# Optimization experiments

Hardware: AMD Instinct MI355X
Metric: run time of the kernel (lower is better)

The kernel has to match this reference:

```python
import jax, jax.numpy as jnp
import numpy as np

BATCH, IN_F, OUT_F = 8192, 4096, 4096


def setup_inputs() -> dict:
    key = jax.random.key(0)
    kx, kw = jax.random.split(key)
    x = jax.random.normal(kx, (BATCH, IN_F), dtype=jnp.float32)
    # weights binarized to {-1, +1} as in __init__ (uniform(-1,1) then sign)
    W = jnp.where(jax.random.normal(kw, (OUT_F, IN_F)) > 0, 1.0, -1.0).astype(jnp.float32)
    return {"x": x, "W": W}


def reference(x, W):
    # forward: input thresholded to {0,1} (x>0 -> 1, else 0), then x_bin @ W^T, no bias
    x_bin = (x > 0).astype(x.dtype)
    return jnp.matmul(x_bin, W.T)  # [batch, out_features]
```

## Files before the change

kernel.cpp:

```cpp
#include <hip/hip_runtime.h>
#include <stdint.h>

typedef __attribute__((ext_vector_type(4))) int v4i;

#define BATCH 8192
#define KDIM  4096
#define NOUT  4096

__global__ __launch_bounds__(256) void pack_x(const float* __restrict__ x,
                                              uint32_t* __restrict__ xb) {
    int t = blockIdx.x * 256 + threadIdx.x;
    float4 f = ((const float4*)x)[t];
    uint32_t b = (f.x > 0.f ? 1u : 0u)
               | ((f.y > 0.f ? 1u : 0u) << 8)
               | ((f.z > 0.f ? 1u : 0u) << 16)
               | ((f.w > 0.f ? 1u : 0u) << 24);
    xb[t] = b;
}

__global__ __launch_bounds__(256) void pack_w(const float* __restrict__ w,
                                              uint32_t* __restrict__ wb) {
    int t = blockIdx.x * 256 + threadIdx.x;
    float4 f = ((const float4*)w)[t];
    uint32_t b = (f.x > 0.f ? 0x01u : 0xFFu)
               | ((f.y > 0.f ? 0x01u : 0xFFu) << 8)
               | ((f.z > 0.f ? 0x01u : 0xFFu) << 16)
               | ((f.w > 0.f ? 0x01u : 0xFFu) << 24);
    wb[t] = b;
}

__global__ __launch_bounds__(256) void bin_gemm(const int8_t* __restrict__ A,
                                                const int8_t* __restrict__ B,
                                                float* __restrict__ C) {
    __shared__ __align__(16) int8_t smA[128 * 64];
    __shared__ __align__(16) int8_t smB[128 * 64];

    const int tid  = threadIdx.x;
    const int w    = tid >> 6;
    const int lane = tid & 63;
    const int q    = lane >> 4;
    const int mp   = lane & 15;

    const int Mbase = blockIdx.y * 128;
    const int Nbase = blockIdx.x * 128;
    const int wm = (w >> 1) * 64;
    const int wn = (w & 1) * 64;

    const int srow = lane >> 2;
    const int swz  = ((lane & 3) ^ ((lane >> 3) & 3)) * 16;
    const int g0   = (w * 2 + 0) * 16;
    const int g1   = (w * 2 + 1) * 16;

    const int8_t* gA0 = A + (size_t)(Mbase + g0 + srow) * KDIM + swz;
    const int8_t* gA1 = A + (size_t)(Mbase + g1 + srow) * KDIM + swz;
    const int8_t* gB0 = B + (size_t)(Nbase + g0 + srow) * KDIM + swz;
    const int8_t* gB1 = B + (size_t)(Nbase + g1 + srow) * KDIM + swz;

    auto lA0 = (__attribute__((address_space(3))) void*)(smA + g0 * 64);
    auto lA1 = (__attribute__((address_space(3))) void*)(smA + g1 * 64);
    auto lB0 = (__attribute__((address_space(3))) void*)(smB + g0 * 64);
    auto lB1 = (__attribute__((address_space(3))) void*)(smB + g1 * 64);

    const int slot = (q ^ ((mp >> 1) & 3)) * 16;

    v4i acc[4][4] = {};

    for (int kt = 0; kt < KDIM / 64; ++kt) {
        const int kof = kt * 64;
        __builtin_amdgcn_global_load_lds(
            (__attribute__((address_space(1))) void*)(gA0 + kof), lA0, 16, 0, 0);
        __builtin_amdgcn_global_load_lds(
            (__attribute__((address_space(1))) void*)(gA1 + kof), lA1, 16, 0, 0);
        __builtin_amdgcn_global_load_lds(
            (__attribute__((address_space(1))) void*)(gB0 + kof), lB0, 16, 0, 0);
        __builtin_amdgcn_global_load_lds(
            (__attribute__((address_space(1))) void*)(gB1 + kof), lB1, 16, 0, 0);
        __syncthreads();

        v4i af[4], bf[4];
        #pragma unroll
        for (int i = 0; i < 4; ++i)
            af[i] = *(const v4i*)(smA + (wm + i * 16 + mp) * 64 + slot);
        #pragma unroll
        for (int i = 0; i < 4; ++i)
            bf[i] = *(const v4i*)(smB + (wn + i * 16 + mp) * 64 + slot);

        #pragma unroll
        for (int mi = 0; mi < 4; ++mi)
            #pragma unroll
            for (int ni = 0; ni < 4; ++ni)
                acc[mi][ni] = __builtin_amdgcn_mfma_i32_16x16x64_i8(
                    af[mi], bf[ni], acc[mi][ni], 0, 0, 0);
        __syncthreads();
    }

    float* Cp = C + (size_t)(Mbase + wm + q * 4) * NOUT + (Nbase + wn + mp);
    #pragma unroll
    for (int mi = 0; mi < 4; ++mi)
        #pragma unroll
        for (int ni = 0; ni < 4; ++ni)
            #pragma unroll
            for (int r = 0; r < 4; ++r)
                Cp[(size_t)(mi * 16 + r) * NOUT + ni * 16] = (float)acc[mi][ni][r];
}

extern "C" void kernel_launch(void* const* d_in, const int* in_sizes, int n_in,
                              void* d_out, int out_size, void* d_ws, size_t ws_size,
                              hipStream_t stream) {
    const float* x = (const float*)d_in[0];
    const float* W = (const float*)d_in[1];
    float* out = (float*)d_out;

    int8_t* xb = (int8_t*)d_ws;
    int8_t* wb = (int8_t*)d_ws + (size_t)BATCH * KDIM;

    pack_x<<<(BATCH * (size_t)KDIM / 4) / 256, 256, 0, stream>>>(x, (uint32_t*)xb);
    pack_w<<<((size_t)NOUT * KDIM / 4) / 256, 256, 0, stream>>>(W, (uint32_t*)wb);

    dim3 grid(NOUT / 128, BATCH / 128);
    bin_gemm<<<grid, 256, 0, stream>>>(xb, wb, out);
}
```

Measured before the change: 398.1 us.

## Switch binary GEMM from int8 MFMA to FP4 scaled MFMA with nibble packing

Inputs and weights are packed as 4-bit FP4 (E2M1) codes instead of int8: x becomes 1.0 or 0 and W becomes ±1.0. The GEMM uses the scaled f8f6f4 MFMA at 16x16x128 in FP4 mode with unit scales and an fp32 accumulator. This halves packed-operand bytes and doubles K per MFMA instruction, so the main loop runs half as many iterations. Exactness depends on fp32 accumulation of integer sums up to 4096, which stays exact, and on the nibble ordering matching what the MFMA expects for its operand layout.

```diff
diff --git a/kernel.cpp b/kernel.cpp
--- a/kernel.cpp
+++ b/kernel.cpp
@@ -1,39 +1,54 @@
 #include <hip/hip_runtime.h>
 #include <stdint.h>
 
-typedef __attribute__((ext_vector_type(4))) int v4i;
+typedef __attribute__((ext_vector_type(4))) int   v4i;
+typedef __attribute__((ext_vector_type(8))) int   v8i;
+typedef __attribute__((ext_vector_type(4))) float v4f;
 
 #define BATCH 8192
 #define KDIM  4096
 #define NOUT  4096
+#define KB    (KDIM / 2)
 
-__global__ __launch_bounds__(256) void pack_x(const float* __restrict__ x,
-                                              uint32_t* __restrict__ xb) {
+__global__ __launch_bounds__(256) void pack_x4(const float* __restrict__ x,
+                                               uint32_t* __restrict__ xb) {
     int t = blockIdx.x * 256 + threadIdx.x;
-    float4 f = ((const float4*)x)[t];
-    uint32_t b = (f.x > 0.f ? 1u : 0u)
-               | ((f.y > 0.f ? 1u : 0u) << 8)
-               | ((f.z > 0.f ? 1u : 0u) << 16)
-               | ((f.w > 0.f ? 1u : 0u) << 24);
+    const float4* p = (const float4*)x + (size_t)t * 2;
+    float4 f0 = p[0];
+    float4 f1 = p[1];
+    uint32_t b = (f0.x > 0.f ? 0x2u        : 0u)
+               | (f0.y > 0.f ? 0x20u       : 0u)
+               | (f0.z > 0.f ? 0x200u      : 0u)
+               | (f0.w > 0.f ? 0x2000u     : 0u)
+               | (f1.x > 0.f ? 0x20000u    : 0u)
+               | (f1.y > 0.f ? 0x200000u   : 0u)
+               | (f1.z > 0.f ? 0x2000000u  : 0u)
+               | (f1.w > 0.f ? 0x20000000u : 0u);
     xb[t] = b;
 }
 
-__global__ __launch_bounds__(256) void pack_w(const float* __restrict__ w,
-                                              uint32_t* __restrict__ wb) {
+__global__ __launch_bounds__(256) void pack_w4(const float* __restrict__ w,
+                                               uint32_t* __restrict__ wb) {
     int t = blockIdx.x * 256 + threadIdx.x;
-    float4 f = ((const float4*)w)[t];
-    uint32_t b = (f.x > 0.f ? 0x01u : 0xFFu)
-               | ((f.y > 0.f ? 0x01u : 0xFFu) << 8)
-               | ((f.z > 0.f ? 0x01u : 0xFFu) << 16)
-               | ((f.w > 0.f ? 0x01u : 0xFFu) << 24);
+    const float4* p = (const float4*)w + (size_t)t * 2;
+    float4 f0 = p[0];
+    float4 f1 = p[1];
+    uint32_t b = (f0.x > 0.f ? 0x2u        : 0xAu)
+               | (f0.y > 0.f ? 0x20u       : 0xA0u)
+               | (f0.z > 0.f ? 0x200u      : 0xA00u)
+               | (f0.w > 0.f ? 0x2000u     : 0xA000u)
+               | (f1.x > 0.f ? 0x20000u    : 0xA0000u)
+               | (f1.y > 0.f ? 0x200000u   : 0xA00000u)
+               | (f1.z > 0.f ? 0x2000000u  : 0xA000000u)
+               | (f1.w > 0.f ? 0x20000000u : 0xA0000000u);
     wb[t] = b;
 }
 
-__global__ __launch_bounds__(256) void bin_gemm(const int8_t* __restrict__ A,
-                                                const int8_t* __restrict__ B,
-                                                float* __restrict__ C) {
-    __shared__ __align__(16) int8_t smA[128 * 64];
-    __shared__ __align__(16) int8_t smB[128 * 64];
+__global__ __launch_bounds__(256) void bin_gemm4(const uint8_t* __restrict__ A,
+                                                 const uint8_t* __restrict__ B,
+                                                 float* __restrict__ C) {
+    __shared__ __align__(16) uint8_t smA[128 * 64];
+    __shared__ __align__(16) uint8_t smB[128 * 64];
 
     const int tid  = threadIdx.x;
     const int w    = tid >> 6;
@@ -51,10 +66,10 @@
     const int g0   = (w * 2 + 0) * 16;
     const int g1   = (w * 2 + 1) * 16;
 
-    const int8_t* gA0 = A + (size_t)(Mbase + g0 + srow) * KDIM + swz;
-    const int8_t* gA1 = A + (size_t)(Mbase + g1 + srow) * KDIM + swz;
-    const int8_t* gB0 = B + (size_t)(Nbase + g0 + srow) * KDIM + swz;
-    const int8_t* gB1 = B + (size_t)(Nbase + g1 + srow) * KDIM + swz;
+    const uint8_t* gA0 = A + (size_t)(Mbase + g0 + srow) * KB + swz;
+    const uint8_t* gA1 = A + (size_t)(Mbase + g1 + srow) * KB + swz;
+    const uint8_t* gB0 = B + (size_t)(Nbase + g0 + srow) * KB + swz;
+    const uint8_t* gB1 = B + (size_t)(Nbase + g1 + srow) * KB + swz;
 
     auto lA0 = (__attribute__((address_space(3))) void*)(smA + g0 * 64);
     auto lA1 = (__attribute__((address_space(3))) void*)(smA + g1 * 64);
@@ -63,9 +78,9 @@
 
     const int slot = (q ^ ((mp >> 1) & 3)) * 16;
 
-    v4i acc[4][4] = {};
+    v4f acc[4][4] = {};
 
-    for (int kt = 0; kt < KDIM / 64; ++kt) {
+    for (int kt = 0; kt < KDIM / 128; ++kt) {
         const int kof = kt * 64;
         __builtin_amdgcn_global_load_lds(
             (__attribute__((address_space(1))) void*)(gA0 + kof), lA0, 16, 0, 0);
@@ -86,11 +101,16 @@
             bf[i] = *(const v4i*)(smB + (wn + i * 16 + mp) * 64 + slot);
 
         #pragma unroll
-        for (int mi = 0; mi < 4; ++mi)
+        for (int mi = 0; mi < 4; ++mi) {
+            v8i a8 = {af[mi][0], af[mi][1], af[mi][2], af[mi][3], 0, 0, 0, 0};
             #pragma unroll
-            for (int ni = 0; ni < 4; ++ni)
-                acc[mi][ni] = __builtin_amdgcn_mfma_i32_16x16x64_i8(
-                    af[mi], bf[ni], acc[mi][ni], 0, 0, 0);
+            for (int ni = 0; ni < 4; ++ni) {
+                v8i b8 = {bf[ni][0], bf[ni][1], bf[ni][2], bf[ni][3], 0, 0, 0, 0};
+                acc[mi][ni] = __builtin_amdgcn_mfma_scale_f32_16x16x128_f8f6f4(
+                    a8, b8, acc[mi][ni], 4, 4,
+                    0, 0x7F7F7F7F, 0, 0x7F7F7F7F);
+            }
+        }
         __syncthreads();
     }
 
@@ -101,7 +121,7 @@
         for (int ni = 0; ni < 4; ++ni)
             #pragma unroll
             for (int r = 0; r < 4; ++r)
-                Cp[(size_t)(mi * 16 + r) * NOUT + ni * 16] = (float)acc[mi][ni][r];
+                Cp[(size_t)(mi * 16 + r) * NOUT + ni * 16] = acc[mi][ni][r];
 }
 
 extern "C" void kernel_launch(void* const* d_in, const int* in_sizes, int n_in,
@@ -111,12 +131,12 @@
     const float* W = (const float*)d_in[1];
     float* out = (float*)d_out;
 
-    int8_t* xb = (int8_t*)d_ws;
-    int8_t* wb = (int8_t*)d_ws + (size_t)BATCH * KDIM;
+    uint8_t* xb = (uint8_t*)d_ws;
+    uint8_t* wb = (uint8_t*)d_ws + (size_t)BATCH * KDIM / 2;
 
-    pack_x<<<(BATCH * (size_t)KDIM / 4) / 256, 256, 0, stream>>>(x, (uint32_t*)xb);
-    pack_w<<<((size_t)NOUT * KDIM / 4) / 256, 256, 0, stream>>>(W, (uint32_t*)wb);
+    pack_x4<<<(BATCH * (size_t)KDIM / 8) / 256, 256, 0, stream>>>(x, (uint32_t*)xb);
+    pack_w4<<<((size_t)NOUT * KDIM / 8) / 256, 256, 0, stream>>>(W, (uint32_t*)wb);
 
     dim3 grid(NOUT / 128, BATCH / 128);
-    bin_gemm<<<grid, 256, 0, stream>>>(xb, wb, out);
+    bin_gemm4<<<grid, 256, 0, stream>>>(xb, wb, out);
 }
```

Measured after the change: 333.1 us. 1.2x faster.
